# Performance work log

Hardware: AMD Instinct MI355X
Metric: run time of the kernel (lower is better)

The kernel has to match this reference:

```python
import jax, jax.numpy as jnp
import numpy as np

IN_DIM = 512
HID = 512
NUM_PARENTS = 200000


def setup_inputs() -> dict:
    key = jax.random.key(0)
    k0, k1, k2, k3, k4 = jax.random.split(key, 5)
    s = 1.0 / np.sqrt(HID)
    return {
        "parent_states": jax.random.normal(k0, (NUM_PARENTS, IN_DIM), dtype=jnp.float32),
        # torch.nn.GRUCell parameters: weight_ih (3H, D), weight_hh (3H, H), biases (3H,)
        "weight_ih": jax.random.uniform(k1, (3 * HID, IN_DIM), minval=-s, maxval=s, dtype=jnp.float32),
        "weight_hh": jax.random.uniform(k2, (3 * HID, HID), minval=-s, maxval=s, dtype=jnp.float32),
        "bias_ih": jax.random.uniform(k3, (3 * HID,), minval=-s, maxval=s, dtype=jnp.float32),
        "bias_hh": jax.random.uniform(k4, (3 * HID,), minval=-s, maxval=s, dtype=jnp.float32),
    }


def reference(parent_states, weight_ih, weight_hh, bias_ih, bias_hh):
    # 1) permutation-invariant aggregation of parent states (mean)
    agg = jnp.mean(parent_states, axis=0)  # (IN_DIM,)
    # 2) GRUCell update with hx = zeros (torch GRUCell default when hx is None)
    h = jnp.zeros((HID,), dtype=parent_states.dtype)
    gi = weight_ih @ agg + bias_ih          # (3H,)
    gh = weight_hh @ h + bias_hh            # (3H,) -> just bias_hh since h=0
    gi_r, gi_z, gi_n = jnp.split(gi, 3)
    gh_r, gh_z, gh_n = jnp.split(gh, 3)
    r = jax.nn.sigmoid(gi_r + gh_r)
    z = jax.nn.sigmoid(gi_z + gh_z)
    n = jnp.tanh(gi_n + r * gh_n)
    h_new = (1.0 - z) * n + z * h           # (HID,)
    return h_new
```

## Files before the change

### kernel.cpp

```cpp
#include <hip/hip_runtime.h>
#include <math.h>

#define IN_DIM 512
#define HID 512

#define K1_BLOCKS 1024
#define K1_THREADS 256
#define K1_STRIDE (K1_BLOCKS * K1_THREADS)
#define P1 K1_BLOCKS
#define K2_BLOCKS 64
#define P2 K2_BLOCKS

__global__ __launch_bounds__(K1_THREADS) void k1_partial(const float* __restrict__ x,
                                                         float* __restrict__ part,
                                                         int total4) {
    const int gtid = blockIdx.x * K1_THREADS + threadIdx.x;
    const float4* __restrict__ x4 = (const float4*)x;
    float4 acc = make_float4(0.f, 0.f, 0.f, 0.f);
    for (int i = gtid; i < total4; i += K1_STRIDE) {
        float4 v = x4[i];
        acc.x += v.x; acc.y += v.y; acc.z += v.z; acc.w += v.w;
    }
    __shared__ float4 lds[K1_THREADS];
    lds[threadIdx.x] = acc;
    __syncthreads();
    if (threadIdx.x < 128) {
        float4 a = lds[threadIdx.x];
        float4 b = lds[threadIdx.x + 128];
        float4 s = make_float4(a.x + b.x, a.y + b.y, a.z + b.z, a.w + b.w);
        ((float4*)(part + (size_t)blockIdx.x * IN_DIM))[threadIdx.x] = s;
    }
}

__global__ __launch_bounds__(IN_DIM) void k2_reduce(const float* __restrict__ part,
                                                    float* __restrict__ part2) {
    const int j = threadIdx.x;
    const int g = blockIdx.x;
    float s = 0.f;
    const int rows = P1 / P2;
    const float* __restrict__ base = part + (size_t)g * rows * IN_DIM + j;
    for (int r = 0; r < rows; ++r) s += base[(size_t)r * IN_DIM];
    part2[(size_t)g * IN_DIM + j] = s;
}

__global__ __launch_bounds__(256) void k3_gemv_gates(const float* __restrict__ part2,
                                                     const float* __restrict__ wih,
                                                     const float* __restrict__ bih,
                                                     const float* __restrict__ bhh,
                                                     float* __restrict__ out,
                                                     float inv_n) {
    __shared__ float agg[IN_DIM];
    for (int c = threadIdx.x; c < IN_DIM; c += 256) {
        float s = 0.f;
        for (int r = 0; r < P2; ++r) s += part2[(size_t)r * IN_DIM + c];
        agg[c] = s * inv_n;
    }
    __syncthreads();

    const int w = threadIdx.x >> 6;
    const int l = threadIdx.x & 63;
    const int j = blockIdx.x * 4 + w;

    const float4* __restrict__ a4 = (const float4*)agg;
    float4 g1 = a4[l];
    float4 g2 = a4[l + 64];

    float d[3];
#pragma unroll
    for (int gidx = 0; gidx < 3; ++gidx) {
        const float4* __restrict__ w4 =
            (const float4*)(wih + (size_t)(gidx * HID + j) * IN_DIM);
        float4 w1 = w4[l];
        float4 w2 = w4[l + 64];
        d[gidx] = w1.x * g1.x + w1.y * g1.y + w1.z * g1.z + w1.w * g1.w
                + w2.x * g2.x + w2.y * g2.y + w2.z * g2.z + w2.w * g2.w;
    }

#pragma unroll
    for (int off = 32; off > 0; off >>= 1) {
        d[0] += __shfl_down(d[0], off, 64);
        d[1] += __shfl_down(d[1], off, 64);
        d[2] += __shfl_down(d[2], off, 64);
    }

    if (l == 0) {
        float gi_r = d[0] + bih[j];
        float gi_z = d[1] + bih[HID + j];
        float gi_n = d[2] + bih[2 * HID + j];
        float gh_r = bhh[j];
        float gh_z = bhh[HID + j];
        float gh_n = bhh[2 * HID + j];
        float r = 1.f / (1.f + expf(-(gi_r + gh_r)));
        float z = 1.f / (1.f + expf(-(gi_z + gh_z)));
        float n = tanhf(gi_n + r * gh_n);
        out[j] = (1.f - z) * n;
    }
}

extern "C" void kernel_launch(void* const* d_in, const int* in_sizes, int n_in,
                              void* d_out, int out_size, void* d_ws, size_t ws_size,
                              hipStream_t stream) {
    const float* x   = (const float*)d_in[0];
    const float* wih = (const float*)d_in[1];
    const float* bih = (const float*)d_in[3];
    const float* bhh = (const float*)d_in[4];
    float* out = (float*)d_out;

    const int n_par  = in_sizes[0] / IN_DIM;
    const int total4 = in_sizes[0] / 4;

    float* part  = (float*)d_ws;
    float* part2 = part + (size_t)P1 * IN_DIM;

    k1_partial<<<K1_BLOCKS, K1_THREADS, 0, stream>>>(x, part, total4);
    k2_reduce<<<K2_BLOCKS, IN_DIM, 0, stream>>>(part, part2);
    k3_gemv_gates<<<HID / 4, 256, 0, stream>>>(part2, wih, bih, bhh, out,
                                               1.0f / (float)n_par);
}
```

Before: 526.0 us.

## Drop intermediate reduce kernel and fold partial sums into gemv kernel

The first-stage reduction now uses 256 blocks of 1024 threads instead of 1024 blocks of 256, so it produces fewer partial rows. The separate second-stage reduce kernel is removed. Each gemv block now sums the 256 partial rows itself, using four accumulators. This saves one kernel launch and one global round trip, but every one of the 128 gemv blocks redundantly re-reads the full partial buffer, and the main pass has fewer blocks to hide memory latency.

Result: slower. 547.2 us (+4.0%).

```diff
diff --git a/kernel.cpp b/kernel.cpp
--- a/kernel.cpp
+++ b/kernel.cpp
@@ -4,46 +4,38 @@
 #define IN_DIM 512
 #define HID 512
 
-#define K1_BLOCKS 1024
-#define K1_THREADS 256
+#define K1_BLOCKS 256
+#define K1_THREADS 1024
 #define K1_STRIDE (K1_BLOCKS * K1_THREADS)
 #define P1 K1_BLOCKS
-#define K2_BLOCKS 64
-#define P2 K2_BLOCKS
+
+__device__ inline float4 f4add(float4 a, float4 b) {
+    return make_float4(a.x + b.x, a.y + b.y, a.z + b.z, a.w + b.w);
+}
 
 __global__ __launch_bounds__(K1_THREADS) void k1_partial(const float* __restrict__ x,
                                                          float* __restrict__ part,
                                                          int total4) {
-    const int gtid = blockIdx.x * K1_THREADS + threadIdx.x;
+    const int t = threadIdx.x;
+    const int gtid = blockIdx.x * K1_THREADS + t;
     const float4* __restrict__ x4 = (const float4*)x;
     float4 acc = make_float4(0.f, 0.f, 0.f, 0.f);
-    for (int i = gtid; i < total4; i += K1_STRIDE) {
-        float4 v = x4[i];
-        acc.x += v.x; acc.y += v.y; acc.z += v.z; acc.w += v.w;
-    }
+    for (int i = gtid; i < total4; i += K1_STRIDE) acc = f4add(acc, x4[i]);
+
     __shared__ float4 lds[K1_THREADS];
-    lds[threadIdx.x] = acc;
+    lds[t] = acc;
     __syncthreads();
-    if (threadIdx.x < 128) {
-        float4 a = lds[threadIdx.x];
-        float4 b = lds[threadIdx.x + 128];
-        float4 s = make_float4(a.x + b.x, a.y + b.y, a.z + b.z, a.w + b.w);
-        ((float4*)(part + (size_t)blockIdx.x * IN_DIM))[threadIdx.x] = s;
+    if (t < 512) lds[t] = f4add(lds[t], lds[t + 512]);
+    __syncthreads();
+    if (t < 256) lds[t] = f4add(lds[t], lds[t + 256]);
+    __syncthreads();
+    if (t < 128) {
+        float4 s = f4add(lds[t], lds[t + 128]);
+        ((float4*)(part + (size_t)blockIdx.x * IN_DIM))[t] = s;
     }
 }
 
-__global__ __launch_bounds__(IN_DIM) void k2_reduce(const float* __restrict__ part,
-                                                    float* __restrict__ part2) {
-    const int j = threadIdx.x;
-    const int g = blockIdx.x;
-    float s = 0.f;
-    const int rows = P1 / P2;
-    const float* __restrict__ base = part + (size_t)g * rows * IN_DIM + j;
-    for (int r = 0; r < rows; ++r) s += base[(size_t)r * IN_DIM];
-    part2[(size_t)g * IN_DIM + j] = s;
-}
-
-__global__ __launch_bounds__(256) void k3_gemv_gates(const float* __restrict__ part2,
+__global__ __launch_bounds__(256) void k2_gemv_gates(const float* __restrict__ part,
                                                      const float* __restrict__ wih,
                                                      const float* __restrict__ bih,
                                                      const float* __restrict__ bhh,
@@ -51,9 +43,16 @@
                                                      float inv_n) {
     __shared__ float agg[IN_DIM];
     for (int c = threadIdx.x; c < IN_DIM; c += 256) {
-        float s = 0.f;
-        for (int r = 0; r < P2; ++r) s += part2[(size_t)r * IN_DIM + c];
-        agg[c] = s * inv_n;
+        float s0 = 0.f, s1 = 0.f, s2 = 0.f, s3 = 0.f;
+        const float* __restrict__ base = part + c;
+#pragma unroll 4
+        for (int r = 0; r < P1; r += 4) {
+            s0 += base[(size_t)(r + 0) * IN_DIM];
+            s1 += base[(size_t)(r + 1) * IN_DIM];
+            s2 += base[(size_t)(r + 2) * IN_DIM];
+            s3 += base[(size_t)(r + 3) * IN_DIM];
+        }
+        agg[c] = ((s0 + s1) + (s2 + s3)) * inv_n;
     }
     __syncthreads();
 
@@ -87,12 +86,9 @@
         float gi_r = d[0] + bih[j];
         float gi_z = d[1] + bih[HID + j];
         float gi_n = d[2] + bih[2 * HID + j];
-        float gh_r = bhh[j];
-        float gh_z = bhh[HID + j];
-        float gh_n = bhh[2 * HID + j];
-        float r = 1.f / (1.f + expf(-(gi_r + gh_r)));
-        float z = 1.f / (1.f + expf(-(gi_z + gh_z)));
-        float n = tanhf(gi_n + r * gh_n);
+        float r = 1.f / (1.f + expf(-(gi_r + bhh[j])));
+        float z = 1.f / (1.f + expf(-(gi_z + bhh[HID + j])));
+        float n = tanhf(gi_n + r * bhh[2 * HID + j]);
         out[j] = (1.f - z) * n;
     }
 }
@@ -109,11 +105,9 @@
     const int n_par  = in_sizes[0] / IN_DIM;
     const int total4 = in_sizes[0] / 4;
 
-    float* part  = (float*)d_ws;
-    float* part2 = part + (size_t)P1 * IN_DIM;
+    float* part = (float*)d_ws;
 
     k1_partial<<<K1_BLOCKS, K1_THREADS, 0, stream>>>(x, part, total4);
-    k2_reduce<<<K2_BLOCKS, IN_DIM, 0, stream>>>(part, part2);
-    k3_gemv_gates<<<HID / 4, 256, 0, stream>>>(part2, wih, bih, bhh, out,
+    k2_gemv_gates<<<HID / 4, 256, 0, stream>>>(part, wih, bih, bhh, out,
                                                1.0f / (float)n_par);
 }
```
